# Optimization experiments

Measured on AMD Instinct MI355X. Metric: run time of the kernel, lower is better.

## Reference

```python
import jax, jax.numpy as jnp
import numpy as np

N_NODES = 100000
N_EDGES = 1600000
D_IN = 128
D_H = 128
N_CLASSES = 64


def setup_inputs() -> dict:
    key = jax.random.key(0)
    ks = jax.random.split(key, 8)
    feat = jax.random.normal(ks[0], (N_NODES, D_IN), dtype=jnp.float32)
    src = jax.random.randint(ks[1], (N_EDGES,), 0, N_NODES)
    dst = jax.random.randint(ks[2], (N_EDGES,), 0, N_NODES)
    # Xavier-ish scaled weights (nn.Linear layout: [out, in])
    W1 = jax.random.normal(ks[3], (D_H, D_IN), dtype=jnp.float32) * (1.0 / np.sqrt(D_IN))
    b1 = jnp.zeros((D_H,), dtype=jnp.float32)
    W2 = jax.random.normal(ks[4], (D_H, D_H), dtype=jnp.float32) * (1.0 / np.sqrt(D_H))
    b2 = jnp.zeros((D_H,), dtype=jnp.float32)
    Wl = jax.random.normal(ks[5], (N_CLASSES, 2 * D_H), dtype=jnp.float32) * (1.0 / np.sqrt(2 * D_H))
    bl = jnp.zeros((N_CLASSES,), dtype=jnp.float32)
    return {"feat": feat, "src": src, "dst": dst, "W1": W1, "b1": b1,
            "W2": W2, "b2": b2, "Wl": Wl, "bl": bl}


def _mean_agg(h, src, dst, inv_deg, n):
    # copy_u('h','m') + mean('m','neigh'): gather src features, segment-sum on dst, divide by in-degree
    s = jax.ops.segment_sum(h[src], dst, num_segments=n)  # [N, D]
    return s * inv_deg


def reference(feat, src, dst, W1, b1, W2, b2, Wl, bl):
    n = feat.shape[0]
    deg = jax.ops.segment_sum(jnp.ones_like(dst, dtype=feat.dtype), dst, num_segments=n)
    inv_deg = (1.0 / jnp.maximum(deg, 1.0))[:, None]  # zero-degree nodes -> 0 (sum is 0 anyway)
    h1 = jax.nn.relu(_mean_agg(feat, src, dst, inv_deg, n) @ W1.T + b1)
    h2 = jax.nn.relu(_mean_agg(h1, src, dst, inv_deg, n) @ W2.T + b2)
    logits = jnp.concatenate([h1, h2], axis=-1) @ Wl.T + bl
    return jax.nn.log_softmax(logits, axis=-1)
```

## Files before the change

kernel.cpp:

```cpp
#include <hip/hip_runtime.h>
#include <hip/hip_fp8.h>
#include <stdint.h>

#define D 128
#define NCLS 64
#define BSH 7
#define NBMAX 1024
#define CCHUNK 4096

typedef __bf16 bf16x8 __attribute__((ext_vector_type(8)));
typedef float f32x4 __attribute__((ext_vector_type(4)));
typedef float f32x2 __attribute__((ext_vector_type(2)));

union B8 { uint4 u; bf16x8 v; };

__device__ __forceinline__ B8 pack8(const float4& a, const float4& b) {
  union { __bf16 h[8]; uint4 u; } p;
  p.h[0] = (__bf16)a.x; p.h[1] = (__bf16)a.y; p.h[2] = (__bf16)a.z; p.h[3] = (__bf16)a.w;
  p.h[4] = (__bf16)b.x; p.h[5] = (__bf16)b.y; p.h[6] = (__bf16)b.z; p.h[7] = (__bf16)b.w;
  B8 r; r.u = p.u; return r;
}


__global__ __launch_bounds__(256) void k_bhist(const int* __restrict__ dst,
                                               int* __restrict__ bcnt, int E, int NB) {
  __shared__ int h[NBMAX];
  for (int i = threadIdx.x; i < NB; i += 256) h[i] = 0;
  __syncthreads();
  for (int e = blockIdx.x * 256 + threadIdx.x; e < E; e += gridDim.x * 256)
    atomicAdd(&h[dst[e] >> BSH], 1);
  __syncthreads();
  for (int i = threadIdx.x; i < NB; i += 256) {
    int c = h[i];
    if (c) atomicAdd(&bcnt[i], c);
  }
}

__global__ __launch_bounds__(1024) void k_bscan(const int* __restrict__ bcnt,
                                                int* __restrict__ bbase,
                                                int* __restrict__ bcur, int NB, int E) {
  __shared__ int sm[NBMAX];
  const int tid = threadIdx.x;
  int v = (tid < NB) ? bcnt[tid] : 0;
  sm[tid] = v;
  __syncthreads();
  for (int off = 1; off < NBMAX; off <<= 1) {
    int t = (tid >= off) ? sm[tid - off] : 0;
    __syncthreads();
    sm[tid] += t;
    __syncthreads();
  }
  if (tid < NB) {
    bbase[tid] = sm[tid] - v;
    bcur[tid] = sm[tid] - v;
  }
  if (tid == 0) bbase[NB] = E;
}

__global__ __launch_bounds__(256) void k_bscatter(const int* __restrict__ src,
                                                  const int* __restrict__ dst,
                                                  int* __restrict__ bcur,
                                                  int* __restrict__ ebuck, int E, int NB) {
  __shared__ int h[NBMAX];
  __shared__ int base[NBMAX];
  const int beg = blockIdx.x * CCHUNK;
  const int end = min(beg + CCHUNK, E);
  for (int i = threadIdx.x; i < NB; i += 256) h[i] = 0;
  __syncthreads();
  for (int e = beg + threadIdx.x; e < end; e += 256)
    atomicAdd(&h[dst[e] >> BSH], 1);
  __syncthreads();
  for (int i = threadIdx.x; i < NB; i += 256) {
    int c = h[i];
    base[i] = c ? atomicAdd(&bcur[i], c) : 0;
    h[i] = 0;
  }
  __syncthreads();
  for (int e = beg + threadIdx.x; e < end; e += 256) {
    const int d = dst[e];
    const int b = d >> BSH;
    const int r = atomicAdd(&h[b], 1);
    ebuck[base[b] + r] = (src[e] << BSH) | (d & 127);
  }
}

__global__ __launch_bounds__(256) void k_bbuild(const int* __restrict__ ebuck,
                                                const int* __restrict__ bbase,
                                                int* __restrict__ row_ptr,
                                                int* __restrict__ esrc,
                                                float* __restrict__ inv, int N, int E) {
  __shared__ int cnt[128], s[128], cur[128];
  const int b = blockIdx.x;
  const int n0 = b << BSH;
  const int nn = min(128, N - n0);
  const int beg = bbase[b], end = bbase[b + 1];
  const int tid = threadIdx.x;
  if (tid < 128) cnt[tid] = 0;
  __syncthreads();
  for (int e = beg + tid; e < end; e += 256)
    atomicAdd(&cnt[ebuck[e] & 127], 1);
  __syncthreads();
  if (tid < 128) s[tid] = cnt[tid];
  __syncthreads();
  for (int off = 1; off < 128; off <<= 1) {
    int t = (tid < 128 && tid >= off) ? s[tid - off] : 0;
    __syncthreads();
    if (tid < 128) s[tid] += t;
    __syncthreads();
  }
  if (tid < 128) {
    const int ex = s[tid] - cnt[tid];
    cur[tid] = ex;
    if (tid < nn) {
      row_ptr[n0 + tid] = beg + ex;
      inv[n0 + tid] = 1.0f / fmaxf((float)cnt[tid], 1.0f);
    }
  }
  if (b == 0 && tid == 0) row_ptr[N] = E;
  __syncthreads();
  for (int e = beg + tid; e < end; e += 256) {
    const int p = ebuck[e];
    const int r = atomicAdd(&cur[p & 127], 1);
    esrc[beg + r] = p >> BSH;
  }
}


__global__ __launch_bounds__(256) void k_gemmz1(const float* __restrict__ A,
                                                const float* __restrict__ W,
                                                unsigned char* __restrict__ Z, int N) {
  const int wave = threadIdx.x >> 6;
  const int lane = threadIdx.x & 63;
  const int l15 = lane & 15;
  const int quad = lane >> 4;

  B8 bfrag[2][4];
#pragma unroll
  for (int t = 0; t < 2; ++t) {
    const int n = wave * 32 + t * 16 + l15;
    const float* wp = W + (size_t)n * D + quad * 8;
#pragma unroll
    for (int ks = 0; ks < 4; ++ks)
      bfrag[t][ks] = pack8(*reinterpret_cast<const float4*>(wp + ks * 32),
                           *reinterpret_cast<const float4*>(wp + ks * 32 + 4));
  }

  const int mtiles = (N + 15) >> 4;
  for (int mt = blockIdx.x; mt < mtiles; mt += gridDim.x) {
    const int arow = min(mt * 16 + l15, N - 1);
    const float* ap = A + (size_t)arow * D + quad * 8;
    B8 a[4];
#pragma unroll
    for (int ks = 0; ks < 4; ++ks)
      a[ks] = pack8(*reinterpret_cast<const float4*>(ap + ks * 32),
                    *reinterpret_cast<const float4*>(ap + ks * 32 + 4));
#pragma unroll
    for (int t = 0; t < 2; ++t) {
      f32x4 acc = {0.f, 0.f, 0.f, 0.f};
#pragma unroll
      for (int ks = 0; ks < 4; ++ks)
        acc = __builtin_amdgcn_mfma_f32_16x16x32_bf16(a[ks].v, bfrag[t][ks].v, acc, 0, 0, 0);
      const int col = wave * 32 + t * 16 + l15;
#pragma unroll
      for (int r = 0; r < 4; ++r) {
        const int orow = mt * 16 + quad * 4 + r;
        if (orow < N) {
          __hip_fp8_e4m3 q((float)acc[r]);
          Z[(size_t)orow * D + col] = q.__x;
        }
      }
    }
  }
}


__global__ __launch_bounds__(256) void k_gemmz2(const ushort* __restrict__ A,
                                                const float* __restrict__ W,
                                                unsigned char* __restrict__ Z, int N) {
  const int wave = threadIdx.x >> 6;
  const int lane = threadIdx.x & 63;
  const int l15 = lane & 15;
  const int quad = lane >> 4;

  B8 bfrag[2][4];
#pragma unroll
  for (int t = 0; t < 2; ++t) {
    const int n = wave * 32 + t * 16 + l15;
    const float* wp = W + (size_t)n * D + quad * 8;
#pragma unroll
    for (int ks = 0; ks < 4; ++ks)
      bfrag[t][ks] = pack8(*reinterpret_cast<const float4*>(wp + ks * 32),
                           *reinterpret_cast<const float4*>(wp + ks * 32 + 4));
  }

  const int mtiles = (N + 15) >> 4;
  for (int mt = blockIdx.x; mt < mtiles; mt += gridDim.x) {
    const int arow = min(mt * 16 + l15, N - 1);
    const ushort* ap = A + (size_t)arow * D + quad * 8;
    B8 a[4];
#pragma unroll
    for (int ks = 0; ks < 4; ++ks)
      a[ks].u = *reinterpret_cast<const uint4*>(ap + ks * 32);
#pragma unroll
    for (int t = 0; t < 2; ++t) {
      f32x4 acc = {0.f, 0.f, 0.f, 0.f};
#pragma unroll
      for (int ks = 0; ks < 4; ++ks)
        acc = __builtin_amdgcn_mfma_f32_16x16x32_bf16(a[ks].v, bfrag[t][ks].v, acc, 0, 0, 0);
      const int col = wave * 32 + t * 16 + l15;
#pragma unroll
      for (int r = 0; r < 4; ++r) {
        const int orow = mt * 16 + quad * 4 + r;
        if (orow < N) {
          __hip_fp8_e4m3 q((float)acc[r]);
          Z[(size_t)orow * D + col] = q.__x;
        }
      }
    }
  }
}


__device__ __forceinline__ void accq8(f32x2 acc[4], const uint2& u) {
  union { uint2 v; unsigned char b[8]; } t;
  t.v = u;
#pragma unroll
  for (int i = 0; i < 4; ++i) {
    __hip_fp8_e4m3 f0, f1;
    f0.__x = t.b[2 * i];
    f1.__x = t.b[2 * i + 1];
    f32x2 d;
    d.x = (float)f0;
    d.y = (float)f1;
    acc[i] += d;
  }
}

__device__ __forceinline__ void gather_acc8(const unsigned char* __restrict__ hp,
                                            const int* __restrict__ esrc,
                                            int beg, int end, f32x2 acc[4]) {
  int e = beg;
  for (; e + 3 < end; e += 4) {
    const int4 ss = *reinterpret_cast<const int4*>(esrc + e);
    const uint2 u0 = *reinterpret_cast<const uint2*>(hp + (size_t)ss.x * D);
    const uint2 u1 = *reinterpret_cast<const uint2*>(hp + (size_t)ss.y * D);
    const uint2 u2 = *reinterpret_cast<const uint2*>(hp + (size_t)ss.z * D);
    const uint2 u3 = *reinterpret_cast<const uint2*>(hp + (size_t)ss.w * D);
    accq8(acc, u0);
    accq8(acc, u1);
    accq8(acc, u2);
    accq8(acc, u3);
  }
  for (; e < end; ++e) {
    const int s0 = esrc[e];
    const uint2 u0 = *reinterpret_cast<const uint2*>(hp + (size_t)s0 * D);
    accq8(acc, u0);
  }
}


__global__ __launch_bounds__(256) void k_gather_relu(const unsigned char* __restrict__ z,
                                                     const int* __restrict__ row_ptr,
                                                     const int* __restrict__ esrc,
                                                     const float* __restrict__ inv,
                                                     const float* __restrict__ bias,
                                                     ushort* __restrict__ out, int N) {
  const int g = threadIdx.x >> 4;
  const int w = threadIdx.x & 15;
  const unsigned char* hp = z + w * 8;
  float bb[8];
  {
    const float4 x = *reinterpret_cast<const float4*>(bias + w * 8);
    const float4 y = *reinterpret_cast<const float4*>(bias + w * 8 + 4);
    bb[0] = x.x; bb[1] = x.y; bb[2] = x.z; bb[3] = x.w;
    bb[4] = y.x; bb[5] = y.y; bb[6] = y.z; bb[7] = y.w;
  }
  const int ntiles = (N + 15) >> 4;
  for (int tile = blockIdx.x; tile < ntiles; tile += gridDim.x) {
    const int node = tile * 16 + g;
    if (node >= N) continue;
    f32x2 acc[4] = {{0.f, 0.f}, {0.f, 0.f}, {0.f, 0.f}, {0.f, 0.f}};
    gather_acc8(hp, esrc, row_ptr[node], row_ptr[node + 1], acc);
    const float iv = inv[node];
    union { __bf16 b[8]; uint4 u; } p;
#pragma unroll
    for (int i = 0; i < 4; ++i) {
      p.b[i * 2 + 0] = (__bf16)fmaxf(acc[i].x * iv + bb[i * 2 + 0], 0.f);
      p.b[i * 2 + 1] = (__bf16)fmaxf(acc[i].y * iv + bb[i * 2 + 1], 0.f);
    }
    *reinterpret_cast<uint4*>(out + (size_t)node * D + w * 8) = p.u;
  }
}


__global__ __launch_bounds__(256) void k_logits(const ushort* __restrict__ h1,
                                                const ushort* __restrict__ h2,
                                                const float* __restrict__ Wl,
                                                const float* __restrict__ bl,
                                                float* __restrict__ out, int N) {
  __shared__ float L[16][NCLS + 4];
  const int wave = threadIdx.x >> 6;
  const int lane = threadIdx.x & 63;
  const int l15 = lane & 15;
  const int quad = lane >> 4;

  B8 bfragL[8];
  const int nlc = wave * 16 + l15;
  const float bbl = bl[nlc];
  {
    const float* wp = Wl + (size_t)nlc * (2 * D) + quad * 8;
#pragma unroll
    for (int ks = 0; ks < 8; ++ks)
      bfragL[ks] = pack8(*reinterpret_cast<const float4*>(wp + ks * 32),
                         *reinterpret_cast<const float4*>(wp + ks * 32 + 4));
  }

  const int mtiles = (N + 15) >> 4;
  for (int mt = blockIdx.x; mt < mtiles; mt += gridDim.x) {
    const int arow = min(mt * 16 + l15, N - 1);
    const ushort* p1 = h1 + (size_t)arow * D + quad * 8;
    const ushort* p2 = h2 + (size_t)arow * D + quad * 8;
    f32x4 acc = {0.f, 0.f, 0.f, 0.f};
    B8 a;
#pragma unroll
    for (int ks = 0; ks < 4; ++ks) {
      a.u = *reinterpret_cast<const uint4*>(p1 + ks * 32);
      acc = __builtin_amdgcn_mfma_f32_16x16x32_bf16(a.v, bfragL[ks].v, acc, 0, 0, 0);
    }
#pragma unroll
    for (int ks = 0; ks < 4; ++ks) {
      a.u = *reinterpret_cast<const uint4*>(p2 + ks * 32);
      acc = __builtin_amdgcn_mfma_f32_16x16x32_bf16(a.v, bfragL[4 + ks].v, acc, 0, 0, 0);
    }
#pragma unroll
    for (int r = 0; r < 4; ++r)
      L[quad * 4 + r][wave * 16 + l15] = acc[r] + bbl;
    __syncthreads();
#pragma unroll
    for (int r = 0; r < 4; ++r) {
      const int row = wave * 4 + r;
      float v = L[row][lane];
      float m = v;
#pragma unroll
      for (int off = 32; off > 0; off >>= 1) m = fmaxf(m, __shfl_xor(m, off));
      float e = __expf(v - m);
#pragma unroll
      for (int off = 32; off > 0; off >>= 1) e += __shfl_xor(e, off);
      const int orow = mt * 16 + row;
      if (orow < N) out[(size_t)orow * NCLS + lane] = v - m - __logf(e);
    }
    __syncthreads();
  }
}


extern "C" void kernel_launch(void* const* d_in, const int* in_sizes, int n_in,
                              void* d_out, int out_size, void* d_ws, size_t ws_size,
                              hipStream_t stream) {
  const float* feat = (const float*)d_in[0];
  const int* src = (const int*)d_in[1];
  const int* dst = (const int*)d_in[2];
  const float* W1 = (const float*)d_in[3];
  const float* b1 = (const float*)d_in[4];
  const float* W2 = (const float*)d_in[5];
  const float* b2 = (const float*)d_in[6];
  const float* Wl = (const float*)d_in[7];
  const float* bl = (const float*)d_in[8];
  float* out = (float*)d_out;

  const int N = in_sizes[0] / D;
  const int E = in_sizes[1];
  const int NB = (N + 127) >> BSH;

  float* ws = (float*)d_ws;
  float* inv = ws;
  ushort* h1b = (ushort*)(inv + N);
  ushort* h2b = h1b + (size_t)N * D;
  unsigned char* z8 = (unsigned char*)(h2b + (size_t)N * D);
  int* row_ptr = (int*)(z8 + (size_t)N * D);
  int* esrc = row_ptr + N + 1;
  int* bcnt = esrc + E;
  int* bbase = bcnt + NBMAX;
  int* bcur = bbase + NBMAX + 1;
  int* ebuck = (int*)z8;

  hipMemsetAsync(bcnt, 0, NBMAX * sizeof(int), stream);

  k_bhist<<<256, 256, 0, stream>>>(dst, bcnt, E, NB);
  k_bscan<<<1, 1024, 0, stream>>>(bcnt, bbase, bcur, NB, E);
  k_bscatter<<<(E + CCHUNK - 1) / CCHUNK, 256, 0, stream>>>(src, dst, bcur, ebuck, E, NB);
  k_bbuild<<<NB, 256, 0, stream>>>(ebuck, bbase, row_ptr, esrc, inv, N, E);

  k_gemmz1<<<2048, 256, 0, stream>>>(feat, W1, z8, N);
  k_gather_relu<<<2048, 256, 0, stream>>>(z8, row_ptr, esrc, inv, b1, h1b, N);

  k_gemmz2<<<2048, 256, 0, stream>>>(h1b, W2, z8, N);
  k_gather_relu<<<2048, 256, 0, stream>>>(z8, row_ptr, esrc, inv, b2, h2b, N);
  k_logits<<<2048, 256, 0, stream>>>(h1b, h2b, Wl, bl, out, N);
}
```

Measured before the change: 389.8 us.

## Fuse degree histogram with first GEMM and make logits per-wave with register softmax

Merges the destination histogram and the first feature GEMM into one launch, with separate block ranges for each, so the two independent stages run concurrently. The edge bucket buffer gets its own workspace region, since it can no longer alias the fp8 GEMM output. The logits kernel now has each wave compute all 64 classes for a 16-row tile. The log-softmax is done with in-register shuffles instead of shared memory and block barriers, and the grid shrinks with launch bounds hinting at 2 blocks. This costs a larger workspace and more registers in the logits kernel.

```diff
diff --git a/kernel.cpp b/kernel.cpp
--- a/kernel.cpp
+++ b/kernel.cpp
@@ -7,6 +7,8 @@
 #define BSH 7
 #define NBMAX 1024
 #define CCHUNK 4096
+#define HISTB 256
+#define GEMMB 2048
 
 typedef __bf16 bf16x8 __attribute__((ext_vector_type(8)));
 typedef float f32x4 __attribute__((ext_vector_type(4)));
@@ -22,19 +24,70 @@
 }
 
 
-__global__ __launch_bounds__(256) void k_bhist(const int* __restrict__ dst,
-                                               int* __restrict__ bcnt, int E, int NB) {
+__global__ __launch_bounds__(256) void k_pre(const int* __restrict__ dst,
+                                             const float* __restrict__ feat,
+                                             const float* __restrict__ W1,
+                                             int* __restrict__ bcnt,
+                                             unsigned char* __restrict__ Z,
+                                             int N, int E, int NB) {
   __shared__ int h[NBMAX];
-  for (int i = threadIdx.x; i < NB; i += 256) h[i] = 0;
-  __syncthreads();
-  for (int e = blockIdx.x * 256 + threadIdx.x; e < E; e += gridDim.x * 256)
-    atomicAdd(&h[dst[e] >> BSH], 1);
-  __syncthreads();
-  for (int i = threadIdx.x; i < NB; i += 256) {
-    int c = h[i];
-    if (c) atomicAdd(&bcnt[i], c);
-  }
-}
+  if (blockIdx.x < HISTB) {
+    for (int i = threadIdx.x; i < NB; i += 256) h[i] = 0;
+    __syncthreads();
+    for (int e = blockIdx.x * 256 + threadIdx.x; e < E; e += HISTB * 256)
+      atomicAdd(&h[dst[e] >> BSH], 1);
+    __syncthreads();
+    for (int i = threadIdx.x; i < NB; i += 256) {
+      int c = h[i];
+      if (c) atomicAdd(&bcnt[i], c);
+    }
+    return;
+  }
+  const int bid = blockIdx.x - HISTB;
+  const int wave = threadIdx.x >> 6;
+  const int lane = threadIdx.x & 63;
+  const int l15 = lane & 15;
+  const int quad = lane >> 4;
+
+  B8 bfrag[2][4];
+#pragma unroll
+  for (int t = 0; t < 2; ++t) {
+    const int n = wave * 32 + t * 16 + l15;
+    const float* wp = W1 + (size_t)n * D + quad * 8;
+#pragma unroll
+    for (int ks = 0; ks < 4; ++ks)
+      bfrag[t][ks] = pack8(*reinterpret_cast<const float4*>(wp + ks * 32),
+                           *reinterpret_cast<const float4*>(wp + ks * 32 + 4));
+  }
+
+  const int mtiles = (N + 15) >> 4;
+  for (int mt = bid; mt < mtiles; mt += GEMMB) {
+    const int arow = min(mt * 16 + l15, N - 1);
+    const float* ap = feat + (size_t)arow * D + quad * 8;
+    B8 a[4];
+#pragma unroll
+    for (int ks = 0; ks < 4; ++ks)
+      a[ks] = pack8(*reinterpret_cast<const float4*>(ap + ks * 32),
+                    *reinterpret_cast<const float4*>(ap + ks * 32 + 4));
+#pragma unroll
+    for (int t = 0; t < 2; ++t) {
+      f32x4 acc = {0.f, 0.f, 0.f, 0.f};
+#pragma unroll
+      for (int ks = 0; ks < 4; ++ks)
+        acc = __builtin_amdgcn_mfma_f32_16x16x32_bf16(a[ks].v, bfrag[t][ks].v, acc, 0, 0, 0);
+      const int col = wave * 32 + t * 16 + l15;
+#pragma unroll
+      for (int r = 0; r < 4; ++r) {
+        const int orow = mt * 16 + quad * 4 + r;
+        if (orow < N) {
+          __hip_fp8_e4m3 q((float)acc[r]);
+          Z[(size_t)orow * D + col] = q.__x;
+        }
+      }
+    }
+  }
+}
+
 
 __global__ __launch_bounds__(1024) void k_bscan(const int* __restrict__ bcnt,
                                                 int* __restrict__ bbase,
@@ -122,54 +175,6 @@
     const int p = ebuck[e];
     const int r = atomicAdd(&cur[p & 127], 1);
     esrc[beg + r] = p >> BSH;
-  }
-}
-
-
-__global__ __launch_bounds__(256) void k_gemmz1(const float* __restrict__ A,
-                                                const float* __restrict__ W,
-                                                unsigned char* __restrict__ Z, int N) {
-  const int wave = threadIdx.x >> 6;
-  const int lane = threadIdx.x & 63;
-  const int l15 = lane & 15;
-  const int quad = lane >> 4;
-
-  B8 bfrag[2][4];
-#pragma unroll
-  for (int t = 0; t < 2; ++t) {
-    const int n = wave * 32 + t * 16 + l15;
-    const float* wp = W + (size_t)n * D + quad * 8;
-#pragma unroll
-    for (int ks = 0; ks < 4; ++ks)
-      bfrag[t][ks] = pack8(*reinterpret_cast<const float4*>(wp + ks * 32),
-                           *reinterpret_cast<const float4*>(wp + ks * 32 + 4));
-  }
-
-  const int mtiles = (N + 15) >> 4;
-  for (int mt = blockIdx.x; mt < mtiles; mt += gridDim.x) {
-    const int arow = min(mt * 16 + l15, N - 1);
-    const float* ap = A + (size_t)arow * D + quad * 8;
-    B8 a[4];
-#pragma unroll
-    for (int ks = 0; ks < 4; ++ks)
-      a[ks] = pack8(*reinterpret_cast<const float4*>(ap + ks * 32),
-                    *reinterpret_cast<const float4*>(ap + ks * 32 + 4));
-#pragma unroll
-    for (int t = 0; t < 2; ++t) {
-      f32x4 acc = {0.f, 0.f, 0.f, 0.f};
-#pragma unroll
-      for (int ks = 0; ks < 4; ++ks)
-        acc = __builtin_amdgcn_mfma_f32_16x16x32_bf16(a[ks].v, bfrag[t][ks].v, acc, 0, 0, 0);
-      const int col = wave * 32 + t * 16 + l15;
-#pragma unroll
-      for (int r = 0; r < 4; ++r) {
-        const int orow = mt * 16 + quad * 4 + r;
-        if (orow < N) {
-          __hip_fp8_e4m3 q((float)acc[r]);
-          Z[(size_t)orow * D + col] = q.__x;
-        }
-      }
-    }
   }
 }
 
@@ -293,63 +298,79 @@
 }
 
 
-__global__ __launch_bounds__(256) void k_logits(const ushort* __restrict__ h1,
-                                                const ushort* __restrict__ h2,
-                                                const float* __restrict__ Wl,
-                                                const float* __restrict__ bl,
-                                                float* __restrict__ out, int N) {
-  __shared__ float L[16][NCLS + 4];
-  const int wave = threadIdx.x >> 6;
+__global__ __launch_bounds__(256, 2) void k_logits(const ushort* __restrict__ h1,
+                                                   const ushort* __restrict__ h2,
+                                                   const float* __restrict__ Wl,
+                                                   const float* __restrict__ bl,
+                                                   float* __restrict__ out, int N) {
   const int lane = threadIdx.x & 63;
   const int l15 = lane & 15;
   const int quad = lane >> 4;
-
-  B8 bfragL[8];
-  const int nlc = wave * 16 + l15;
-  const float bbl = bl[nlc];
-  {
-    const float* wp = Wl + (size_t)nlc * (2 * D) + quad * 8;
+  const int wid = blockIdx.x * 4 + (threadIdx.x >> 6);
+  const int nw = gridDim.x * 4;
+
+  B8 wfrag[4][8];
+  float blv[4];
+#pragma unroll
+  for (int t = 0; t < 4; ++t) {
+    const int n = t * 16 + l15;
+    blv[t] = bl[n];
+    const float* wp = Wl + (size_t)n * (2 * D) + quad * 8;
 #pragma unroll
     for (int ks = 0; ks < 8; ++ks)
-      bfragL[ks] = pack8(*reinterpret_cast<const float4*>(wp + ks * 32),
-                         *reinterpret_cast<const float4*>(wp + ks * 32 + 4));
+      wfrag[t][ks] = pack8(*reinterpret_cast<const float4*>(wp + ks * 32),
+                           *reinterpret_cast<const float4*>(wp + ks * 32 + 4));
   }
 
   const int mtiles = (N + 15) >> 4;
-  for (int mt = blockIdx.x; mt < mtiles; mt += gridDim.x) {
+  for (int mt = wid; mt < mtiles; mt += nw) {
     const int arow = min(mt * 16 + l15, N - 1);
     const ushort* p1 = h1 + (size_t)arow * D + quad * 8;
     const ushort* p2 = h2 + (size_t)arow * D + quad * 8;
-    f32x4 acc = {0.f, 0.f, 0.f, 0.f};
-    B8 a;
+    B8 a1[4], a2[4];
 #pragma unroll
     for (int ks = 0; ks < 4; ++ks) {
-      a.u = *reinterpret_cast<const uint4*>(p1 + ks * 32);
-      acc = __builtin_amdgcn_mfma_f32_16x16x32_bf16(a.v, bfragL[ks].v, acc, 0, 0, 0);
-    }
-#pragma unroll
-    for (int ks = 0; ks < 4; ++ks) {
-      a.u = *reinterpret_cast<const uint4*>(p2 + ks * 32);
-      acc = __builtin_amdgcn_mfma_f32_16x16x32_bf16(a.v, bfragL[4 + ks].v, acc, 0, 0, 0);
-    }
-#pragma unroll
-    for (int r = 0; r < 4; ++r)
-      L[quad * 4 + r][wave * 16 + l15] = acc[r] + bbl;
-    __syncthreads();
+      a1[ks].u = *reinterpret_cast<const uint4*>(p1 + ks * 32);
+      a2[ks].u = *reinterpret_cast<const uint4*>(p2 + ks * 32);
+    }
+    f32x4 acc[4];
+#pragma unroll
+    for (int t = 0; t < 4; ++t) acc[t] = f32x4{0.f, 0.f, 0.f, 0.f};
+#pragma unroll
+    for (int ks = 0; ks < 4; ++ks)
+#pragma unroll
+      for (int t = 0; t < 4; ++t)
+        acc[t] = __builtin_amdgcn_mfma_f32_16x16x32_bf16(a1[ks].v, wfrag[t][ks].v, acc[t], 0, 0, 0);
+#pragma unroll
+    for (int ks = 0; ks < 4; ++ks)
+#pragma unroll
+      for (int t = 0; t < 4; ++t)
+        acc[t] = __builtin_amdgcn_mfma_f32_16x16x32_bf16(a2[ks].v, wfrag[t][4 + ks].v, acc[t], 0, 0, 0);
+#pragma unroll
+    for (int t = 0; t < 4; ++t)
+#pragma unroll
+      for (int r = 0; r < 4; ++r)
+        acc[t][r] += blv[t];
 #pragma unroll
     for (int r = 0; r < 4; ++r) {
-      const int row = wave * 4 + r;
-      float v = L[row][lane];
-      float m = v;
-#pragma unroll
-      for (int off = 32; off > 0; off >>= 1) m = fmaxf(m, __shfl_xor(m, off));
-      float e = __expf(v - m);
-#pragma unroll
-      for (int off = 32; off > 0; off >>= 1) e += __shfl_xor(e, off);
-      const int orow = mt * 16 + row;
-      if (orow < N) out[(size_t)orow * NCLS + lane] = v - m - __logf(e);
-    }
-    __syncthreads();
+      float m = fmaxf(fmaxf(acc[0][r], acc[1][r]), fmaxf(acc[2][r], acc[3][r]));
+#pragma unroll
+      for (int off = 8; off > 0; off >>= 1) m = fmaxf(m, __shfl_xor(m, off));
+      const float e0 = __expf(acc[0][r] - m);
+      const float e1 = __expf(acc[1][r] - m);
+      const float e2 = __expf(acc[2][r] - m);
+      const float e3 = __expf(acc[3][r] - m);
+      float s = (e0 + e1) + (e2 + e3);
+#pragma unroll
+      for (int off = 8; off > 0; off >>= 1) s += __shfl_xor(s, off);
+      const float ls = m + __logf(s);
+      const int orow = mt * 16 + quad * 4 + r;
+      if (orow < N) {
+        float* op = out + (size_t)orow * NCLS + l15;
+#pragma unroll
+        for (int t = 0; t < 4; ++t) op[t * 16] = acc[t][r] - ls;
+      }
+    }
   }
 }
 
@@ -379,22 +400,23 @@
   unsigned char* z8 = (unsigned char*)(h2b + (size_t)N * D);
   int* row_ptr = (int*)(z8 + (size_t)N * D);
   int* esrc = row_ptr + N + 1;
-  int* bcnt = esrc + E;
+  int* ebuck = esrc + E;
+  int* bcnt = ebuck + E;
   int* bbase = bcnt + NBMAX;
   int* bcur = bbase + NBMAX + 1;
-  int* ebuck = (int*)z8;
 
   hipMemsetAsync(bcnt, 0, NBMAX * sizeof(int), stream);
 
-  k_bhist<<<256, 256, 0, stream>>>(dst, bcnt, E, NB);
+  k_pre<<<HISTB + GEMMB, 256, 0, stream>>>(dst, feat, W1, bcnt, z8, N, E, NB);
+
   k_bscan<<<1, 1024, 0, stream>>>(bcnt, bbase, bcur, NB, E);
   k_bscatter<<<(E + CCHUNK - 1) / CCHUNK, 256, 0, stream>>>(src, dst, bcur, ebuck, E, NB);
   k_bbuild<<<NB, 256, 0, stream>>>(ebuck, bbase, row_ptr, esrc, inv, N, E);
 
-  k_gemmz1<<<2048, 256, 0, stream>>>(feat, W1, z8, N);
   k_gather_relu<<<2048, 256, 0, stream>>>(z8, row_ptr, esrc, inv, b1, h1b, N);
 
   k_gemmz2<<<2048, 256, 0, stream>>>(h1b, W2, z8, N);
   k_gather_relu<<<2048, 256, 0, stream>>>(z8, row_ptr, esrc, inv, b2, h2b, N);
-  k_logits<<<2048, 256, 0, stream>>>(h1b, h2b, Wl, bl, out, N);
-}
+
+  k_logits<<<512, 256, 0, stream>>>(h1b, h2b, Wl, bl, out, N);
+}
```

After: 361.7 us. -7.2%, faster.
